# Kernel tuning notes

Hardware: AMD Instinct MI355X
Metric: run time of the kernel (lower is better)

The kernel has to match this reference:

```python
import jax, jax.numpy as jnp
import numpy as np

A1, A2 = 16, 16            # block tile sizes (arr_size1, arr_size2)
G = 1000                   # graph_size (max node index + 1)
EG = 16000                 # number of graph edges (avg degree 16)
SIZE1 = G * A1             # input feature length  (16000)
SIZE2 = G * A2             # output feature length (16000)
NNZ = EG * A1 * A2         # expanded COO entries  (4,096,000)
B = 32                     # batch


def _expand_indices(t0, t1, a1, a2):
    """Vectorized adjust_indices: edge (t0,t1) -> tile of (row,col) pairs.
    row = t0*a2 + j, col = t1*a1 + i  for all i in [a1), j in [a2)."""
    e = t0.shape[0]
    j = np.arange(a2)
    i = np.arange(a1)
    rows = np.broadcast_to(t0[:, None, None] * a2 + j[None, None, :], (e, a1, a2)).reshape(-1)
    cols = np.broadcast_to(t1[:, None, None] * a1 + i[None, :, None], (e, a1, a2)).reshape(-1)
    return rows.astype(np.int32), cols.astype(np.int32)


def setup_inputs() -> dict:
    key = jax.random.key(0)
    ks = jax.random.split(key, 6)
    rng = np.random.default_rng(0)
    t0 = rng.integers(0, G, EG)
    t1 = rng.integers(0, G, EG)
    rows_np, cols_np = _expand_indices(t0, t1, A1, A2)
    # original init: uniform(-1/len(indices), 1/len(indices)) with len([2,nnz])==2 -> U(-0.5, 0.5)
    return {
        "x": jax.random.normal(ks[0], (B, SIZE1, 1), dtype=jnp.float32),
        "weight_mean": jax.random.uniform(ks[1], (NNZ,), jnp.float32, -0.5, 0.5),
        "weight_log_var": jnp.zeros((NNZ,), jnp.float32),
        "b_mean": jax.random.uniform(ks[2], (SIZE2,), jnp.float32, -0.5, 0.5),
        "b_log_var": jnp.zeros((SIZE2,), jnp.float32),
        "eps_w": jax.random.normal(ks[3], (NNZ,), dtype=jnp.float32),
        "eps_b": jax.random.normal(ks[4], (SIZE2,), dtype=jnp.float32),
        "rows": jnp.asarray(rows_np),
        "cols": jnp.asarray(cols_np),
    }


def reference(x, weight_mean, weight_log_var, b_mean, b_log_var, eps_w, eps_b, rows, cols):
    # reparameterization sample of sparse weight values
    values = eps_w * jnp.exp(weight_log_var) + weight_mean          # [NNZ]
    # COO spmm: out[b, r, k] += values[e] * x[b, c, k] for each (r, c) = (rows[e], cols[e])
    contrib = values[None, :, None] * x[:, cols, :]                 # [B, NNZ, 1]
    out = jnp.zeros((x.shape[0], SIZE2, x.shape[2]), x.dtype).at[:, rows, :].add(contrib)
    # reparameterized bias, broadcast over batch
    b = eps_b * jnp.exp(b_log_var) + b_mean                         # [SIZE2]
    out = out + b[None, :, None]
    # kl is explicitly zeroed in the source right before return
    return (out, jnp.asarray(0.0, dtype=x.dtype))
```

## Files before the change

kernel.cpp:

```cpp
#include <hip/hip_runtime.h>

#define EG   16000
#define NG   1000
#define BB   32
#define SIZE 16000
#define CAP  64

typedef float f32x4 __attribute__((ext_vector_type(4)));

__global__ __launch_bounds__(256) void bucket_kernel(
    const int* __restrict__ rows, const int* __restrict__ cols,
    int* __restrict__ cnt, int* __restrict__ bucket)
{
    int e = blockIdx.x * 256 + threadIdx.x;
    if (e < EG) {
        int t0 = rows[(long)e << 8] >> 4;
        int t1 = cols[(long)e << 8] >> 4;
        int pos = atomicAdd(&cnt[t0], 1);
        if (pos < CAP) bucket[t0 * CAP + pos] = (e << 10) | t1;
    }
}

__global__ __launch_bounds__(256) void spmm_kernel(
    const float* __restrict__ wm, const float* __restrict__ wlv,
    const float* __restrict__ ew, const float* __restrict__ x,
    const float* __restrict__ bm, const float* __restrict__ blv,
    const float* __restrict__ eb,
    const int* __restrict__ cnt, const int* __restrict__ bucket,
    float* __restrict__ out)
{
    __shared__ f32x4 vt[2][4][64];
    __shared__ f32x4 xs[2][4][160];
    __shared__ int   sl[CAP];

    int g    = blockIdx.x;
    int tid  = threadIdx.x;
    int wave = tid >> 6;
    int lane = tid & 63;
    int jg   = lane & 3;
    int cb2  = lane >> 2;

    int n = cnt[g]; n = n < CAP ? n : CAP;
    if (tid < n) sl[tid] = bucket[g * CAP + tid];
    __syncthreads();

    f32x4 acc0 = {0.f,0.f,0.f,0.f}, acc1 = {0.f,0.f,0.f,0.f};
    f32x4 m4, l4, g4, xv0, xv1;
    int iters = (n + 3) >> 2;
    bool vcur = false, vnxt = false;

    auto issue = [&](int idx) -> bool {
        bool val = idx < n;
        if (val) {
            int pk = sl[idx];
            int e  = pk >> 10;
            int t1 = pk & 1023;
            long wq = ((long)e << 6) + lane;
            m4 = ((const f32x4*)wm)[wq];
            l4 = ((const f32x4*)wlv)[wq];
            g4 = ((const f32x4*)ew)[wq];
            const f32x4* x4 = (const f32x4*)x;
            int c0 = lane, c1 = lane + 64;
            xv0 = x4[(long)(c0 >> 2) * (SIZE/4) + (t1 << 2) + (c0 & 3)];
            xv1 = x4[(long)(c1 >> 2) * (SIZE/4) + (t1 << 2) + (c1 & 3)];
        }
        return val;
    };
    auto writeb = [&](int buf, bool val) {
        if (val) {
            f32x4 v;
            v.x = g4.x * __expf(l4.x) + m4.x;
            v.y = g4.y * __expf(l4.y) + m4.y;
            v.z = g4.z * __expf(l4.z) + m4.z;
            v.w = g4.w * __expf(l4.w) + m4.w;
            vt[buf][wave][lane] = v;
            int c0 = lane, c1 = lane + 64;
            xs[buf][wave][(c0 >> 2) * 5 + (c0 & 3)] = xv0;
            xs[buf][wave][(c1 >> 2) * 5 + (c1 & 3)] = xv1;
        }
    };
    auto compute = [&](int buf, bool val) {
        if (!val) return;
        f32x4 a0 = xs[buf][wave][ cb2       * 5 + 0];
        f32x4 a1 = xs[buf][wave][ cb2       * 5 + 1];
        f32x4 a2 = xs[buf][wave][ cb2       * 5 + 2];
        f32x4 a3 = xs[buf][wave][ cb2       * 5 + 3];
        f32x4 b0 = xs[buf][wave][(cb2 + 16) * 5 + 0];
        f32x4 b1 = xs[buf][wave][(cb2 + 16) * 5 + 1];
        f32x4 b2 = xs[buf][wave][(cb2 + 16) * 5 + 2];
        f32x4 b3 = xs[buf][wave][(cb2 + 16) * 5 + 3];
        float xra[16] = {a0.x,a0.y,a0.z,a0.w, a1.x,a1.y,a1.z,a1.w,
                         a2.x,a2.y,a2.z,a2.w, a3.x,a3.y,a3.z,a3.w};
        float xrb[16] = {b0.x,b0.y,b0.z,b0.w, b1.x,b1.y,b1.z,b1.w,
                         b2.x,b2.y,b2.z,b2.w, b3.x,b3.y,b3.z,b3.w};
        #pragma unroll
        for (int i = 0; i < 16; ++i) {
            f32x4 w = vt[buf][wave][(i << 2) + jg];
            acc0 += w * xra[i];
            acc1 += w * xrb[i];
        }
    };

    vcur = issue(wave);
    writeb(0, vcur);
    __syncthreads();
    for (int it = 0; it < iters; ++it) {
        bool more = (it + 1 < iters);
        if (more) vnxt = issue(((it + 1) << 2) + wave);
        compute(it & 1, vcur);
        if (more) writeb((it + 1) & 1, vnxt);
        __syncthreads();
        vcur = vnxt;
    }

    f32x4* sred = &xs[0][0][0];
    sred[(wave << 7) + (lane << 1) + 0] = acc0;
    sred[(wave << 7) + (lane << 1) + 1] = acc1;
    __syncthreads();
    if (tid < 128) {
        int cb  = tid >> 2;
        int jgf = tid & 3;
        int h   = cb >> 4;
        int sl_ = ((cb & 15) << 2) + jgf;
        f32x4 s = sred[(0 << 7) + (sl_ << 1) + h]
                + sred[(1 << 7) + (sl_ << 1) + h]
                + sred[(2 << 7) + (sl_ << 1) + h]
                + sred[(3 << 7) + (sl_ << 1) + h];
        int r0 = (g << 4) + (jgf << 2);
        f32x4 b4 = *(const f32x4*)&bm[r0];
        f32x4 v4 = *(const f32x4*)&blv[r0];
        f32x4 e4 = *(const f32x4*)&eb[r0];
        f32x4 o;
        o.x = s.x + (e4.x * __expf(v4.x) + b4.x);
        o.y = s.y + (e4.y * __expf(v4.y) + b4.y);
        o.z = s.z + (e4.z * __expf(v4.z) + b4.z);
        o.w = s.w + (e4.w * __expf(v4.w) + b4.w);
        *(f32x4*)&out[(long)cb * SIZE + r0] = o;
    }
    if (g == 0 && tid == 0) out[(long)BB * SIZE] = 0.0f;
}

extern "C" void kernel_launch(void* const* d_in, const int* in_sizes, int n_in,
                              void* d_out, int out_size, void* d_ws, size_t ws_size,
                              hipStream_t stream) {
    const float* x   = (const float*)d_in[0];
    const float* wm  = (const float*)d_in[1];
    const float* wlv = (const float*)d_in[2];
    const float* bm  = (const float*)d_in[3];
    const float* blv = (const float*)d_in[4];
    const float* ew  = (const float*)d_in[5];
    const float* eb  = (const float*)d_in[6];
    const int* rows  = (const int*)d_in[7];
    const int* cols  = (const int*)d_in[8];
    float* out = (float*)d_out;

    char* ws = (char*)d_ws;
    int* cnt    = (int*)(ws);
    int* bucket = (int*)(ws + 4096);

    hipMemsetAsync(cnt, 0, 4096, stream);
    bucket_kernel<<<(EG + 255) / 256, 256, 0, stream>>>(rows, cols, cnt, bucket);
    spmm_kernel<<<NG, 256, 0, stream>>>(wm, wlv, ew, x, bm, blv, eb,
                                        cnt, bucket, out);
}
```

Measured before the change: 135.0 us.

## Replace global bucketing with per-block shared-memory edge scan, drop memset

Removes the hipMemsetAsync and the global atomic bucketing pass. A pack kernel now writes one packed (t0,t1) word per edge, and each spmm block scans all 16000 packed entries to collect its own edges through shared-memory atomics. This cuts a launch and the global atomics, but every block now reads the full 64KB packed array, which it may mostly hit in cache. Edge order within a bucket still depends on atomic order, so the float summation order can vary between runs. Launch bounds also gain a minimum of 4 blocks per SM.

Result: no change. 133.0 us (-1.5%).

```diff
diff --git a/kernel.cpp b/kernel.cpp
--- a/kernel.cpp
+++ b/kernel.cpp
@@ -8,41 +8,51 @@
 
 typedef float f32x4 __attribute__((ext_vector_type(4)));
 
-__global__ __launch_bounds__(256) void bucket_kernel(
+__global__ __launch_bounds__(256) void pack_kernel(
     const int* __restrict__ rows, const int* __restrict__ cols,
-    int* __restrict__ cnt, int* __restrict__ bucket)
+    int* __restrict__ pk)
 {
     int e = blockIdx.x * 256 + threadIdx.x;
     if (e < EG) {
         int t0 = rows[(long)e << 8] >> 4;
         int t1 = cols[(long)e << 8] >> 4;
-        int pos = atomicAdd(&cnt[t0], 1);
-        if (pos < CAP) bucket[t0 * CAP + pos] = (e << 10) | t1;
+        pk[e] = (t0 << 10) | t1;
     }
 }
 
-__global__ __launch_bounds__(256) void spmm_kernel(
+__global__ __launch_bounds__(256, 4) void spmm_kernel(
     const float* __restrict__ wm, const float* __restrict__ wlv,
     const float* __restrict__ ew, const float* __restrict__ x,
     const float* __restrict__ bm, const float* __restrict__ blv,
-    const float* __restrict__ eb,
-    const int* __restrict__ cnt, const int* __restrict__ bucket,
+    const float* __restrict__ eb, const int* __restrict__ pk,
     float* __restrict__ out)
 {
     __shared__ f32x4 vt[2][4][64];
     __shared__ f32x4 xs[2][4][160];
     __shared__ int   sl[CAP];
+    __shared__ int   scnt;
 
-    int g    = blockIdx.x;
-    int tid  = threadIdx.x;
+    int g   = blockIdx.x;
+    int tid = threadIdx.x;
+
+    if (tid == 0) scnt = 0;
+    __syncthreads();
+    const int4* pk4 = (const int4*)pk;
+    for (int c = tid; c < EG / 4; c += 256) {
+        int4 v = pk4[c];
+        int e0 = c << 2;
+        if ((v.x >> 10) == g) { int p = atomicAdd(&scnt, 1); if (p < CAP) sl[p] = ((e0    ) << 10) | (v.x & 1023); }
+        if ((v.y >> 10) == g) { int p = atomicAdd(&scnt, 1); if (p < CAP) sl[p] = ((e0 + 1) << 10) | (v.y & 1023); }
+        if ((v.z >> 10) == g) { int p = atomicAdd(&scnt, 1); if (p < CAP) sl[p] = ((e0 + 2) << 10) | (v.z & 1023); }
+        if ((v.w >> 10) == g) { int p = atomicAdd(&scnt, 1); if (p < CAP) sl[p] = ((e0 + 3) << 10) | (v.w & 1023); }
+    }
+    __syncthreads();
+    int n = scnt; n = n < CAP ? n : CAP;
+
     int wave = tid >> 6;
     int lane = tid & 63;
     int jg   = lane & 3;
     int cb2  = lane >> 2;
-
-    int n = cnt[g]; n = n < CAP ? n : CAP;
-    if (tid < n) sl[tid] = bucket[g * CAP + tid];
-    __syncthreads();
 
     f32x4 acc0 = {0.f,0.f,0.f,0.f}, acc1 = {0.f,0.f,0.f,0.f};
     f32x4 m4, l4, g4, xv0, xv1;
@@ -52,9 +62,9 @@
     auto issue = [&](int idx) -> bool {
         bool val = idx < n;
         if (val) {
-            int pk = sl[idx];
-            int e  = pk >> 10;
-            int t1 = pk & 1023;
+            int pkv = sl[idx];
+            int e   = pkv >> 10;
+            int t1  = pkv & 1023;
             long wq = ((long)e << 6) + lane;
             m4 = ((const f32x4*)wm)[wq];
             l4 = ((const f32x4*)wlv)[wq];
@@ -154,12 +164,8 @@
     const int* cols  = (const int*)d_in[8];
     float* out = (float*)d_out;
 
-    char* ws = (char*)d_ws;
-    int* cnt    = (int*)(ws);
-    int* bucket = (int*)(ws + 4096);
+    int* pk = (int*)d_ws;
 
-    hipMemsetAsync(cnt, 0, 4096, stream);
-    bucket_kernel<<<(EG + 255) / 256, 256, 0, stream>>>(rows, cols, cnt, bucket);
-    spmm_kernel<<<NG, 256, 0, stream>>>(wm, wlv, ew, x, bm, blv, eb,
-                                        cnt, bucket, out);
+    pack_kernel<<<(EG + 255) / 256, 256, 0, stream>>>(rows, cols, pk);
+    spmm_kernel<<<NG, 256, 0, stream>>>(wm, wlv, ew, x, bm, blv, eb, pk, out);
 }
```
